# Kernel optimization log

Measured on AMD Instinct MI355X. Metric: run time of the kernel, lower is better.

## Reference

```python
import jax, jax.numpy as jnp
import numpy as np

N, T, D, H = 64, 512, 1024, 1024

def setup_inputs() -> dict:
    key = jax.random.key(0)
    k1, k2, k3, k4 = jax.random.split(key, 4)
    x = jax.random.normal(k1, (N, T, D), dtype=jnp.float32)
    h0 = jax.random.normal(k2, (N, H), dtype=jnp.float32)
    Wx = jax.random.normal(k3, (D, H), dtype=jnp.float32) / jnp.sqrt(jnp.float32(D))
    Wh = jax.random.normal(k4, (H, H), dtype=jnp.float32) / jnp.sqrt(jnp.float32(H))
    b = jnp.zeros((H,), dtype=jnp.float32)
    return {"x": x, "h0": h0, "Wx": Wx, "Wh": Wh, "b": b}

def reference(x, h0, Wx, Wh, b):
    # Precompute input projections for all timesteps in one big GEMM: (N,T,D)@(D,H)
    xw = jnp.einsum('ntd,dh->nth', x, Wx) + b  # (N, T, H)

    def step(prev_h, xw_t):
        next_h = jnp.tanh(xw_t + prev_h @ Wh)
        return next_h, next_h

    # scan over time: move T to leading axis
    _, hs = jax.lax.scan(step, h0, jnp.swapaxes(xw, 0, 1))  # hs: (T, N, H)
    return jnp.swapaxes(hs, 0, 1)  # (N, T, H)
```

## Files before the change

kernel.cpp:

```cpp
#include <hip/hip_runtime.h>
#include <hip/hip_bf16.h>
#include <stdint.h>
#include <stddef.h>

typedef short bf16x8 __attribute__((ext_vector_type(8)));
typedef float f32x4 __attribute__((ext_vector_type(4)));
typedef int i32x4 __attribute__((ext_vector_type(4)));
typedef unsigned short u16;
typedef unsigned int u32;
typedef unsigned long long u64;

#define SCOPE_AGENT __HIP_MEMORY_SCOPE_AGENT
#define SENT 0xFFFFFFFFFFFFFFFFull

__device__ __forceinline__ u16 f2bf(float x) {
  u32 u = __builtin_bit_cast(u32, x);
  u32 r = (u + 0x7fffu + ((u >> 16) & 1u)) >> 16;
  return (u16)r;
}
__device__ __forceinline__ float bf2f(u16 h) {
  u32 u = ((u32)h) << 16;
  return __builtin_bit_cast(float, u);
}
__device__ __forceinline__ void split2(float a, float b, u32& hw, u32& lw) {
  u16 ha = f2bf(a), hb = f2bf(b);
  float ra = a - bf2f(ha), rb = b - bf2f(hb);
  hw = (u32)ha | ((u32)hb << 16);
  lw = (u32)f2bf(ra) | ((u32)f2bf(rb) << 16);
}
__device__ __forceinline__ u32 pack_hl(float v) {
  u16 hi = f2bf(v);
  u16 lo = f2bf(v - bf2f(hi));
  return ((u32)hi << 16) | (u32)lo;
}
__device__ __forceinline__ float tanh_fast(float x) {
  float xc = fminf(9.0f, fmaxf(-9.0f, x));
  float z = exp2f(xc * 2.8853900817779268f);
  return (z - 1.0f) * __builtin_amdgcn_rcpf(z + 1.0f);
}

__global__ void wsplit(const float* __restrict__ W, u16* __restrict__ Thi, u16* __restrict__ Tlo) {
  __shared__ float tile[32][33];
  const int bx = blockIdx.x * 32;
  const int by = blockIdx.y * 32;
  const int tx = threadIdx.x, ty = threadIdx.y;
#pragma unroll
  for (int r = 0; r < 4; ++r) {
    int ky = ty + 8 * r;
    tile[ky][tx] = W[(size_t)(by + ky) * 1024 + bx + tx];
  }
  __syncthreads();
#pragma unroll
  for (int r = 0; r < 4; ++r) {
    int row = ty + 8 * r;
    float v = tile[tx][row];
    u16 hi = f2bf(v);
    u16 lo = f2bf(v - bf2f(hi));
    Thi[(size_t)(bx + row) * 1024 + by + tx] = hi;
    Tlo[(size_t)(bx + row) * 1024 + by + tx] = lo;
  }
}

__global__ void hinit(const float* __restrict__ h0, u64* __restrict__ ring) {
  int i = blockIdx.x * 256 + threadIdx.x;
  int slot = i >> 15, li = i & 32767;
  if (slot == 0) {
    int g = li >> 13, I = li & 8191;
    int Bb = I >> 8, rem = I & 255;
    int j2 = rem >> 6, q = (rem >> 4) & 3, row = rem & 15;
    int kp = Bb * 16 + q * 4 + j2, k = kp * 2;
    int n = g * 16 + row;
    u64 val = (u64)pack_hl(h0[n * 1024 + k]) | ((u64)pack_hl(h0[n * 1024 + k + 1]) << 32);
    __hip_atomic_store(&ring[i], val, __ATOMIC_RELAXED, SCOPE_AGENT);
  } else {
    __hip_atomic_store(&ring[i], SENT, __ATOMIC_RELAXED, SCOPE_AGENT);
  }
}

#define LDT 40

__global__ __launch_bounds__(256, 2) void xw_gemm(
    const float* __restrict__ X, const u16* __restrict__ BThi, const u16* __restrict__ BTlo,
    const float* __restrict__ bias, float* __restrict__ out) {
  __shared__ u16 Ah[128 * LDT], Al[128 * LDT], Bh[128 * LDT], Bl[128 * LDT];
  const int tid = threadIdx.x;
  const int lane = tid & 63, wave = tid >> 6;
  const int wm = wave >> 1, wn = wave & 1;
  const int m0 = blockIdx.y * 128, n0 = blockIdx.x * 128;
  const int arow = tid >> 1, afo = (tid & 1) << 4;
  const int bcol = tid >> 1, bko = (tid & 1) << 4;
  const float* Xa = X + (size_t)(m0 + arow) * 1024 + afo;
  const u16* bhp = BThi + (size_t)(n0 + bcol) * 1024 + bko;
  const u16* blp = BTlo + (size_t)(n0 + bcol) * 1024 + bko;

  f32x4 acc[4][4] = {};

  const int aoff = (wm * 64 + (lane & 15)) * LDT + ((lane >> 4) << 3);
  const int boff = (wn * 64 + (lane & 15)) * LDT + ((lane >> 4) << 3);

  for (int k0 = 0; k0 < 1024; k0 += 32) {
    const float4* xp = (const float4*)(Xa + k0);
    float4 f0 = xp[0], f1 = xp[1], f2 = xp[2], f3 = xp[3];
    i32x4 gbh0 = *(const i32x4*)(bhp + k0);
    i32x4 gbh1 = *(const i32x4*)(bhp + k0 + 8);
    i32x4 gbl0 = *(const i32x4*)(blp + k0);
    i32x4 gbl1 = *(const i32x4*)(blp + k0 + 8);
    u32 hw0, hw1, hw2, hw3, hw4, hw5, hw6, hw7;
    u32 lw0, lw1, lw2, lw3, lw4, lw5, lw6, lw7;
    split2(f0.x, f0.y, hw0, lw0); split2(f0.z, f0.w, hw1, lw1);
    split2(f1.x, f1.y, hw2, lw2); split2(f1.z, f1.w, hw3, lw3);
    split2(f2.x, f2.y, hw4, lw4); split2(f2.z, f2.w, hw5, lw5);
    split2(f3.x, f3.y, hw6, lw6); split2(f3.z, f3.w, hw7, lw7);
    __syncthreads();
    *(i32x4*)&Ah[arow * LDT + afo]     = i32x4{(int)hw0, (int)hw1, (int)hw2, (int)hw3};
    *(i32x4*)&Ah[arow * LDT + afo + 8] = i32x4{(int)hw4, (int)hw5, (int)hw6, (int)hw7};
    *(i32x4*)&Al[arow * LDT + afo]     = i32x4{(int)lw0, (int)lw1, (int)lw2, (int)lw3};
    *(i32x4*)&Al[arow * LDT + afo + 8] = i32x4{(int)lw4, (int)lw5, (int)lw6, (int)lw7};
    *(i32x4*)&Bh[bcol * LDT + bko]     = gbh0;
    *(i32x4*)&Bh[bcol * LDT + bko + 8] = gbh1;
    *(i32x4*)&Bl[bcol * LDT + bko]     = gbl0;
    *(i32x4*)&Bl[bcol * LDT + bko + 8] = gbl1;
    __syncthreads();

    bf16x8 a_h[4], a_l[4], b_h[4], b_l[4];
#pragma unroll
    for (int i = 0; i < 4; ++i) {
      a_h[i] = *(const bf16x8*)(Ah + aoff + i * 16 * LDT);
      a_l[i] = *(const bf16x8*)(Al + aoff + i * 16 * LDT);
      b_h[i] = *(const bf16x8*)(Bh + boff + i * 16 * LDT);
      b_l[i] = *(const bf16x8*)(Bl + boff + i * 16 * LDT);
    }
#pragma unroll
    for (int i = 0; i < 4; ++i)
#pragma unroll
      for (int j = 0; j < 4; ++j)
        acc[i][j] = __builtin_amdgcn_mfma_f32_16x16x32_bf16(a_h[i], b_h[j], acc[i][j], 0, 0, 0);
#pragma unroll
    for (int i = 0; i < 4; ++i)
#pragma unroll
      for (int j = 0; j < 4; ++j)
        acc[i][j] = __builtin_amdgcn_mfma_f32_16x16x32_bf16(a_h[i], b_l[j], acc[i][j], 0, 0, 0);
#pragma unroll
    for (int i = 0; i < 4; ++i)
#pragma unroll
      for (int j = 0; j < 4; ++j)
        acc[i][j] = __builtin_amdgcn_mfma_f32_16x16x32_bf16(a_l[i], b_h[j], acc[i][j], 0, 0, 0);
  }
  const int ccol = n0 + wn * 64 + (lane & 15);
  const int crow = m0 + wm * 64 + ((lane >> 4) << 2);
#pragma unroll
  for (int j = 0; j < 4; ++j) {
    float bv = bias[ccol + j * 16];
#pragma unroll
    for (int i = 0; i < 4; ++i)
#pragma unroll
      for (int r = 0; r < 4; ++r)
        out[(size_t)(crow + i * 16 + r) * 1024 + ccol + j * 16] = acc[i][j][r] + bv;
  }
}

#define RST 68

__global__ __launch_bounds__(512, 2) void rnn_scan(
    const u16* __restrict__ WThi, const u16* __restrict__ WTlo,
    float* __restrict__ out, u64* __restrict__ ring) {
  __shared__ float Red[2][8][16 * RST];
  const int tid = threadIdx.x;
  const int lane = tid & 63, w = tid >> 6;
  const int cw = blockIdx.x & 15, g = blockIdx.x >> 4;
  const int colL = lane & 15, q = lane >> 4;

  i32x4 Bh_[4][4], Bl_[4][4];
#pragma unroll
  for (int ct = 0; ct < 4; ++ct) {
    const u16* bhp = WThi + (size_t)(cw * 64 + ct * 16 + colL) * 1024 + w * 128 + (q << 3);
    const u16* blp = WTlo + (size_t)(cw * 64 + ct * 16 + colL) * 1024 + w * 128 + (q << 3);
#pragma unroll
    for (int t = 0; t < 4; ++t) {
      asm volatile("global_load_dwordx4 %0, %1, off" : "=v"(Bh_[ct][t]) : "v"(bhp + t * 32));
      asm volatile("global_load_dwordx4 %0, %1, off" : "=v"(Bl_[ct][t]) : "v"(blp + t * 32));
    }
  }
  asm volatile("s_waitcnt vmcnt(0)" ::: "memory");
  __builtin_amdgcn_sched_barrier(0);

  const int rem = tid & 255;
  const int frow = tid & 15;
  const int kp = (2 * cw + (tid >> 8)) * 16 + ((rem >> 4) & 3) * 4 + (rem >> 6);
  const int colL2 = 2 * (kp - cw * 32);
  const size_t pubI = (size_t)cw * 512 + tid;
  const size_t orow = ((size_t)(g * 16 + frow) * 512) * 1024 + cw * 64 + colL2;
  const size_t gslab = (size_t)g * 8192;
  const size_t srcoff = gslab + (size_t)w * 1024 + lane;

  for (int s = 0; s < 512; ++s) {
    const size_t oidx = orow + (size_t)s * 1024;
    float2 xwv = *(const float2*)&out[oidx];
    asm volatile("" : "+v"(xwv.x), "+v"(xwv.y));

    const u64* src = ring + (size_t)(s & 3) * 32768 + srcoff;
    u64 hv[16];
#pragma unroll
    for (int t = 0; t < 4; ++t)
#pragma unroll
      for (int j2 = 0; j2 < 4; ++j2)
        hv[t * 4 + j2] = __hip_atomic_load(src + t * 256 + j2 * 64, __ATOMIC_RELAXED, SCOPE_AGENT);
    {
      int it = 0;
      while (true) {
        bool d = true;
#pragma unroll
        for (int i = 0; i < 16; ++i) d = d && (hv[i] != SENT);
        if (__all(d) || ++it >= (1 << 16)) break;
#pragma unroll
        for (int t = 0; t < 4; ++t)
#pragma unroll
          for (int j2 = 0; j2 < 4; ++j2)
            if (hv[t * 4 + j2] == SENT)
              hv[t * 4 + j2] =
                  __hip_atomic_load(src + t * 256 + j2 * 64, __ATOMIC_RELAXED, SCOPE_AGENT);
      }
    }

    f32x4 acc[4] = {};
#pragma unroll
    for (int t = 0; t < 4; ++t) {
      u64 w0 = hv[t * 4 + 0], w1 = hv[t * 4 + 1], w2 = hv[t * 4 + 2], w3 = hv[t * 4 + 3];
      i32x4 ahv, alv;
      ahv[0] = (int)__builtin_amdgcn_perm((u32)(w0 >> 32), (u32)w0, 0x07060302u);
      alv[0] = (int)__builtin_amdgcn_perm((u32)(w0 >> 32), (u32)w0, 0x05040100u);
      ahv[1] = (int)__builtin_amdgcn_perm((u32)(w1 >> 32), (u32)w1, 0x07060302u);
      alv[1] = (int)__builtin_amdgcn_perm((u32)(w1 >> 32), (u32)w1, 0x05040100u);
      ahv[2] = (int)__builtin_amdgcn_perm((u32)(w2 >> 32), (u32)w2, 0x07060302u);
      alv[2] = (int)__builtin_amdgcn_perm((u32)(w2 >> 32), (u32)w2, 0x05040100u);
      ahv[3] = (int)__builtin_amdgcn_perm((u32)(w3 >> 32), (u32)w3, 0x07060302u);
      alv[3] = (int)__builtin_amdgcn_perm((u32)(w3 >> 32), (u32)w3, 0x05040100u);
      bf16x8 ah = __builtin_bit_cast(bf16x8, ahv);
      bf16x8 al = __builtin_bit_cast(bf16x8, alv);
#pragma unroll
      for (int ct = 0; ct < 4; ++ct) {
        acc[ct] = __builtin_amdgcn_mfma_f32_16x16x32_bf16(al, __builtin_bit_cast(bf16x8, Bh_[ct][t]), acc[ct], 0, 0, 0);
        acc[ct] = __builtin_amdgcn_mfma_f32_16x16x32_bf16(ah, __builtin_bit_cast(bf16x8, Bl_[ct][t]), acc[ct], 0, 0, 0);
        acc[ct] = __builtin_amdgcn_mfma_f32_16x16x32_bf16(ah, __builtin_bit_cast(bf16x8, Bh_[ct][t]), acc[ct], 0, 0, 0);
      }
    }

#pragma unroll
    for (int ct = 0; ct < 4; ++ct)
#pragma unroll
      for (int r = 0; r < 4; ++r)
        Red[s & 1][w][(q * 4 + r) * RST + ct * 16 + colL] = acc[ct][r];
    __syncthreads();

    float s0 = xwv.x, s1 = xwv.y;
#pragma unroll
    for (int ww = 0; ww < 8; ++ww) {
      float2 pr = *(const float2*)&Red[s & 1][ww][frow * RST + colL2];
      s0 += pr.x; s1 += pr.y;
    }
    float h0v = tanh_fast(s0), h1v = tanh_fast(s1);

    u64 val = (u64)pack_hl(h0v) | ((u64)pack_hl(h1v) << 32);
    __hip_atomic_store(ring + (size_t)((s + 1) & 3) * 32768 + gslab + pubI, val,
                       __ATOMIC_RELAXED, SCOPE_AGENT);
    if (s > 0)
      __hip_atomic_store(ring + (size_t)((s - 1) & 3) * 32768 + gslab + pubI, SENT,
                         __ATOMIC_RELAXED, SCOPE_AGENT);
    *(float2*)&out[oidx] = make_float2(h0v, h1v);
  }
}

extern "C" void kernel_launch(void* const* d_in, const int* in_sizes, int n_in,
                              void* d_out, int out_size, void* d_ws, size_t ws_size,
                              hipStream_t stream) {
  const float* x    = (const float*)d_in[0];
  const float* h0   = (const float*)d_in[1];
  const float* Wx   = (const float*)d_in[2];
  const float* Wh   = (const float*)d_in[3];
  const float* bias = (const float*)d_in[4];
  float* out = (float*)d_out;
  char* ws = (char*)d_ws;

  const size_t MB2 = (size_t)1 << 21;
  u16* WxThi = (u16*)(ws);
  u16* WxTlo = (u16*)(ws + MB2);
  u16* WhThi = (u16*)(ws + 2 * MB2);
  u16* WhTlo = (u16*)(ws + 3 * MB2);
  u64* ring  = (u64*)(ws + 4 * MB2);

  wsplit<<<dim3(32, 32), dim3(32, 8), 0, stream>>>(Wx, WxThi, WxTlo);
  wsplit<<<dim3(32, 32), dim3(32, 8), 0, stream>>>(Wh, WhThi, WhTlo);
  hinit<<<512, 256, 0, stream>>>(h0, ring);
  xw_gemm<<<dim3(8, 256), 256, 0, stream>>>(x, WxThi, WxTlo, bias, out);
  rnn_scan<<<64, 512, 0, stream>>>(WhThi, WhTlo, out, ring);
}
```

Before: 1.869 ms.

## Split RNN scan batch groups to 8 rows, doubling persistent blocks

Result: faster. 1.579 ms, median of 2 (-15.6%).

```diff
diff --git a/kernel.cpp b/kernel.cpp
--- a/kernel.cpp
+++ b/kernel.cpp
@@ -65,11 +65,10 @@
   int i = blockIdx.x * 256 + threadIdx.x;
   int slot = i >> 15, li = i & 32767;
   if (slot == 0) {
-    int g = li >> 13, I = li & 8191;
-    int Bb = I >> 8, rem = I & 255;
-    int j2 = rem >> 6, q = (rem >> 4) & 3, row = rem & 15;
-    int kp = Bb * 16 + q * 4 + j2, k = kp * 2;
-    int n = g * 16 + row;
+    int g = li >> 12, I8 = li & 4095;
+    int row = I8 & 7, q = (I8 >> 3) & 3, j2 = (I8 >> 5) & 3, hi4 = I8 >> 7;
+    int kp = hi4 * 16 + q * 4 + j2, k = kp * 2;
+    int n = g * 8 + row;
     u64 val = (u64)pack_hl(h0[n * 1024 + k]) | ((u64)pack_hl(h0[n * 1024 + k + 1]) << 32);
     __hip_atomic_store(&ring[i], val, __ATOMIC_RELAXED, SCOPE_AGENT);
   } else {
@@ -164,7 +163,7 @@
 __global__ __launch_bounds__(512, 2) void rnn_scan(
     const u16* __restrict__ WThi, const u16* __restrict__ WTlo,
     float* __restrict__ out, u64* __restrict__ ring) {
-  __shared__ float Red[2][8][16 * RST];
+  __shared__ float Red[2][8][8 * RST];
   const int tid = threadIdx.x;
   const int lane = tid & 63, w = tid >> 6;
   const int cw = blockIdx.x & 15, g = blockIdx.x >> 4;
@@ -184,48 +183,59 @@
   asm volatile("s_waitcnt vmcnt(0)" ::: "memory");
   __builtin_amdgcn_sched_barrier(0);
 
-  const int rem = tid & 255;
-  const int frow = tid & 15;
-  const int kp = (2 * cw + (tid >> 8)) * 16 + ((rem >> 4) & 3) * 4 + (rem >> 6);
-  const int colL2 = 2 * (kp - cw * 32);
-  const size_t pubI = (size_t)cw * 512 + tid;
-  const size_t orow = ((size_t)(g * 16 + frow) * 512) * 1024 + cw * 64 + colL2;
-  const size_t gslab = (size_t)g * 8192;
-  const size_t srcoff = gslab + (size_t)w * 1024 + lane;
+  const int frow = tid & 7;
+  const int kloc = 32 * (tid >> 7) + 8 * ((tid >> 3) & 3) + 2 * ((tid >> 5) & 3);
+  const bool fin = tid < 256;
+  const size_t pubI = (size_t)cw * 256 + tid;
+  const size_t orow = ((size_t)(g * 8 + frow) * 512) * 1024 + cw * 64 + kloc;
+  const size_t gslab = (size_t)g * 4096;
+  const int j2o = (colL >> 3) * 2;
+  const size_t srcoff = gslab + (size_t)w * 512 + (q << 3) + (colL & 7);
 
   for (int s = 0; s < 512; ++s) {
     const size_t oidx = orow + (size_t)s * 1024;
-    float2 xwv = *(const float2*)&out[oidx];
-    asm volatile("" : "+v"(xwv.x), "+v"(xwv.y));
+    float2 xwv = make_float2(0.f, 0.f);
+    if (fin) {
+      xwv = *(const float2*)&out[oidx];
+      asm volatile("" : "+v"(xwv.x), "+v"(xwv.y));
+    }
 
     const u64* src = ring + (size_t)(s & 3) * 32768 + srcoff;
-    u64 hv[16];
+    u64 hv[8];
 #pragma unroll
     for (int t = 0; t < 4; ++t)
 #pragma unroll
-      for (int j2 = 0; j2 < 4; ++j2)
-        hv[t * 4 + j2] = __hip_atomic_load(src + t * 256 + j2 * 64, __ATOMIC_RELAXED, SCOPE_AGENT);
+      for (int i = 0; i < 2; ++i)
+        hv[t * 2 + i] =
+            __hip_atomic_load(src + t * 128 + (j2o + i) * 32, __ATOMIC_RELAXED, SCOPE_AGENT);
     {
       int it = 0;
       while (true) {
         bool d = true;
 #pragma unroll
-        for (int i = 0; i < 16; ++i) d = d && (hv[i] != SENT);
+        for (int i = 0; i < 8; ++i) d = d && (hv[i] != SENT);
         if (__all(d) || ++it >= (1 << 16)) break;
 #pragma unroll
         for (int t = 0; t < 4; ++t)
 #pragma unroll
-          for (int j2 = 0; j2 < 4; ++j2)
-            if (hv[t * 4 + j2] == SENT)
-              hv[t * 4 + j2] =
-                  __hip_atomic_load(src + t * 256 + j2 * 64, __ATOMIC_RELAXED, SCOPE_AGENT);
+          for (int i = 0; i < 2; ++i)
+            if (hv[t * 2 + i] == SENT)
+              hv[t * 2 + i] =
+                  __hip_atomic_load(src + t * 128 + (j2o + i) * 32, __ATOMIC_RELAXED, SCOPE_AGENT);
       }
     }
 
+    const bool hi8 = (colL & 8) != 0;
     f32x4 acc[4] = {};
 #pragma unroll
     for (int t = 0; t < 4; ++t) {
-      u64 w0 = hv[t * 4 + 0], w1 = hv[t * 4 + 1], w2 = hv[t * 4 + 2], w3 = hv[t * 4 + 3];
+      u64 a0 = hv[t * 2 + 0], a1 = hv[t * 2 + 1];
+      u64 p0 = __shfl_xor((unsigned long long)a0, 8);
+      u64 p1 = __shfl_xor((unsigned long long)a1, 8);
+      u64 w0 = hi8 ? p0 : a0;
+      u64 w1 = hi8 ? p1 : a1;
+      u64 w2 = hi8 ? a0 : p0;
+      u64 w3 = hi8 ? a1 : p1;
       i32x4 ahv, alv;
       ahv[0] = (int)__builtin_amdgcn_perm((u32)(w0 >> 32), (u32)w0, 0x07060302u);
       alv[0] = (int)__builtin_amdgcn_perm((u32)(w0 >> 32), (u32)w0, 0x05040100u);
@@ -245,28 +255,32 @@
       }
     }
 
-#pragma unroll
-    for (int ct = 0; ct < 4; ++ct)
-#pragma unroll
-      for (int r = 0; r < 4; ++r)
-        Red[s & 1][w][(q * 4 + r) * RST + ct * 16 + colL] = acc[ct][r];
+    if (q < 2) {
+#pragma unroll
+      for (int ct = 0; ct < 4; ++ct)
+#pragma unroll
+        for (int r = 0; r < 4; ++r)
+          Red[s & 1][w][(q * 4 + r) * RST + ct * 16 + colL] = acc[ct][r];
+    }
     __syncthreads();
 
-    float s0 = xwv.x, s1 = xwv.y;
-#pragma unroll
-    for (int ww = 0; ww < 8; ++ww) {
-      float2 pr = *(const float2*)&Red[s & 1][ww][frow * RST + colL2];
-      s0 += pr.x; s1 += pr.y;
-    }
-    float h0v = tanh_fast(s0), h1v = tanh_fast(s1);
-
-    u64 val = (u64)pack_hl(h0v) | ((u64)pack_hl(h1v) << 32);
-    __hip_atomic_store(ring + (size_t)((s + 1) & 3) * 32768 + gslab + pubI, val,
-                       __ATOMIC_RELAXED, SCOPE_AGENT);
-    if (s > 0)
-      __hip_atomic_store(ring + (size_t)((s - 1) & 3) * 32768 + gslab + pubI, SENT,
+    if (fin) {
+      float s0 = xwv.x, s1 = xwv.y;
+#pragma unroll
+      for (int ww = 0; ww < 8; ++ww) {
+        float2 pr = *(const float2*)&Red[s & 1][ww][frow * RST + kloc];
+        s0 += pr.x; s1 += pr.y;
+      }
+      float h0v = tanh_fast(s0), h1v = tanh_fast(s1);
+
+      u64 val = (u64)pack_hl(h0v) | ((u64)pack_hl(h1v) << 32);
+      __hip_atomic_store(ring + (size_t)((s + 1) & 3) * 32768 + gslab + pubI, val,
                          __ATOMIC_RELAXED, SCOPE_AGENT);
-    *(float2*)&out[oidx] = make_float2(h0v, h1v);
+      if (s > 0)
+        __hip_atomic_store(ring + (size_t)((s - 1) & 3) * 32768 + gslab + pubI, SENT,
+                           __ATOMIC_RELAXED, SCOPE_AGENT);
+      *(float2*)&out[oidx] = make_float2(h0v, h1v);
+    }
   }
 }
 
@@ -292,5 +306,5 @@
   wsplit<<<dim3(32, 32), dim3(32, 8), 0, stream>>>(Wh, WhThi, WhTlo);
   hinit<<<512, 256, 0, stream>>>(h0, ring);
   xw_gemm<<<dim3(8, 256), 256, 0, stream>>>(x, WxThi, WxTlo, bias, out);
-  rnn_scan<<<64, 512, 0, stream>>>(WhThi, WhTlo, out, ring);
-}
+  rnn_scan<<<128, 512, 0, stream>>>(WhThi, WhTlo, out, ring);
+}
```
